# Kernel optimization log

Hardware: AMD Instinct MI355X
Metric: run time of the kernel (lower is better)

## Reference

```python
import jax, jax.numpy as jnp
import numpy as np
from jax import lax

BN_EPS = 1e-5

def _conv1d_same(x, w):
    # x: [N, 1, C], w: [1, 1, k] with k odd -> SAME padding along channel axis
    k = w.shape[-1]
    return lax.conv_general_dilated(x, w, window_strides=(1,),
                                    padding=[(k // 2, k // 2)],
                                    dimension_numbers=('NCH', 'OIH', 'NCH'))

def setup_inputs() -> dict:
    key = jax.random.key(0)
    ks = jax.random.split(key, 6)
    B, C, H, W = 4, 64, 64, 64
    kk = 3  # kernel size from in_dim=64: t=int(abs(log2(64)+1)/2)=3 (odd)
    x = jax.random.normal(ks[0], (B, C, H, W), dtype=jnp.float32)
    q_w = jax.random.normal(ks[1], (1, 1, kk), dtype=jnp.float32) * 0.5
    k_w = jax.random.normal(ks[2], (1, 1, kk), dtype=jnp.float32) * 0.5
    v_w = jax.random.normal(ks[3], (C, C), dtype=jnp.float32) * (1.0 / np.sqrt(C))
    v_b = jnp.zeros((C,), dtype=jnp.float32)
    gamma = jax.random.uniform(ks[4], (1,), dtype=jnp.float32, minval=0.5, maxval=1.5)
    bn_w = jnp.ones((C,), dtype=jnp.float32)
    bn_b = jnp.zeros((C,), dtype=jnp.float32)
    return {"x": x, "q_w": q_w, "k_w": k_w, "v_w": v_w, "v_b": v_b,
            "gamma": gamma, "bn_w": bn_w, "bn_b": bn_b}

def reference(x, q_w, k_w, v_w, v_b, gamma, bn_w, bn_b):
    B, C, H, W = x.shape
    N = H * W
    # conv1d Q/K projections over the channel axis, per spatial position
    xp = x.reshape(B, C, N).transpose(0, 2, 1).reshape(B * N, 1, C)
    q = _conv1d_same(xp, q_w).reshape(B, N, C)   # proj_query: [B, HW, C]
    k = _conv1d_same(xp, k_w).reshape(B, N, C)   # proj_key (pre-permute)
    energy = jnp.einsum('bnc,bmc->bnm', q, k)    # [B, HW, HW]
    attn = jax.nn.softmax(energy, axis=-1)
    # 1x1 value conv
    v = jnp.einsum('oc,bchw->bohw', v_w, x) + v_b[None, :, None, None]
    vv = v.reshape(B, C, N)
    # bmm(value, attention^T)
    out = jnp.einsum('bcm,bnm->bcn', vv, attn).reshape(B, C, H, W)
    y = gamma[0] * out
    # BatchNorm2d, training mode (batch statistics, biased variance)
    mean = jnp.mean(y, axis=(0, 2, 3), keepdims=True)
    var = jnp.var(y, axis=(0, 2, 3), keepdims=True)
    y = (y - mean) * lax.rsqrt(var + BN_EPS)
    y = y * bn_w[None, :, None, None] + bn_b[None, :, None, None]
    return y + x
```

## Files before the change

kernel.cpp:

```cpp
#include <hip/hip_runtime.h>
#include <stdint.h>

using f16 = _Float16;

typedef _Float16 f16x8 __attribute__((ext_vector_type(8)));
typedef _Float16 f16x4 __attribute__((ext_vector_type(4)));
typedef float f32x4 __attribute__((ext_vector_type(4)));

#define LOG2E 1.44269504088896340736f

__device__ __forceinline__ f16 f2h(float f) { return (f16)f; }

#if __has_builtin(__builtin_amdgcn_exp2f)
__device__ __forceinline__ float fexp2(float x) { return __builtin_amdgcn_exp2f(x); }
#else
__device__ __forceinline__ float fexp2(float x) { return exp2f(x); }
#endif

typedef __attribute__((address_space(1))) const uint32_t gu32;
typedef __attribute__((address_space(3))) uint32_t lu32;

__device__ __forceinline__ void dma16(const void* g, void* l) {
  __builtin_amdgcn_global_load_lds((gu32*)g, (lu32*)l, 16, 0, 0);
}

__device__ __forceinline__ f16x8 cvt8(const float* p) {
  const float4 a = *(const float4*)p;
  const float4 b = *(const float4*)(p + 4);
  f16x8 r;
  r[0] = (f16)a.x; r[1] = (f16)a.y; r[2] = (f16)a.z; r[3] = (f16)a.w;
  r[4] = (f16)b.x; r[5] = (f16)b.y; r[6] = (f16)b.z; r[7] = (f16)b.w;
  return r;
}


__global__ __launch_bounds__(256, 2) void pam_pre(
    const float* __restrict__ x, const float* __restrict__ qw,
    const float* __restrict__ kw, const float* __restrict__ vw,
    const float* __restrict__ vb,
    f16* __restrict__ qa, f16* __restrict__ ka2, f16* __restrict__ va3,
    float* __restrict__ gz)
{
  __shared__ alignas(16) f16 xt[16 * 72];
  const int tid = threadIdx.x;
  const int b = blockIdx.x >> 8;
  const int n0 = (blockIdx.x & 255) << 4;
  const int lane = tid & 63;
  const int wv = tid >> 6;
  const int quad = lane >> 4, l15 = lane & 15;

  if (blockIdx.x == 0 && tid < 128) gz[tid] = 0.f;

  {
    const int c = tid >> 2;
    const int j0 = (tid & 3) << 2;
    const float4 v0 = *(const float4*)(x + ((size_t)(b * 64 + c) << 12) + n0 + j0);
    xt[(j0 + 0) * 72 + c] = f2h(v0.x);
    xt[(j0 + 1) * 72 + c] = f2h(v0.y);
    xt[(j0 + 2) * 72 + c] = f2h(v0.z);
    xt[(j0 + 3) * 72 + c] = f2h(v0.w);
  }
  __syncthreads();

  const float qw0 = qw[0], qw1 = qw[1], qw2 = qw[2];
  const float kw0 = kw[0], kw1 = kw[1], kw2 = kw[2];
  for (int p = 0; p < 4; ++p) {
    const int c = lane;
    const int jr = (p << 2) + wv;
    const int n = n0 + jr;
    const float xm = (c > 0) ? (float)xt[jr * 72 + c - 1] : 0.f;
    const float x0 = (float)xt[jr * 72 + c];
    const float xp = (c < 63) ? (float)xt[jr * 72 + c + 1] : 0.f;
    const float qv = (qw0 * xm + qw1 * x0 + qw2 * xp) * LOG2E;
    const float kv = kw0 * xm + kw1 * x0 + kw2 * xp;
    qa[((size_t)((b << 12) + n) << 6) + c] = f2h(qv);
    ka2[((size_t)(b * 8 + (c >> 3)) << 15) + (n << 3) + (c & 7)] = f2h(kv);
  }

  {
    const f16x8 a0 = cvt8(vw + (wv * 16 + l15) * 64 + quad * 8);
    const f16x8 a1 = cvt8(vw + (wv * 16 + l15) * 64 + quad * 8 + 32);
    const f16x8 b0 = *(const f16x8*)&xt[l15 * 72 + quad * 8];
    const f16x8 b1 = *(const f16x8*)&xt[l15 * 72 + quad * 8 + 32];
    f32x4 z = {0.f, 0.f, 0.f, 0.f};
    z = __builtin_amdgcn_mfma_f32_16x16x32_f16(a0, b0, z, 0, 0, 0);
    z = __builtin_amdgcn_mfma_f32_16x16x32_f16(a1, b1, z, 0, 0, 0);
    const int cobase = wv * 16 + quad * 4;
    for (int r = 0; r < 4; ++r) {
      const int co = cobase + r;
      const int n = n0 + l15;
      const float val = z[r] + vb[co];
      va3[(((size_t)(b * 1024 + (n >> 2))) << 8) + (co << 2) + (n & 3)] = f2h(val);
    }
  }
}

__global__ __launch_bounds__(512, 2) void pam_attn(
    const f16* __restrict__ qa, const f16* __restrict__ ka2,
    const f16* __restrict__ va3, const float* __restrict__ gam,
    float* __restrict__ y0, float* __restrict__ gs1, float* __restrict__ gs2)
{
  __shared__ alignas(16) f16 kbuf[2][8192];
  __shared__ alignas(16) f16 vbuf[2][8192];
  __shared__ float ldsO[32 * 65];
  __shared__ float ldsM[4][32], ldsL[4][32], ldsMg[32], ldsInv[32];

  const int tid = threadIdx.x;
  const int wv = tid >> 6, lane = tid & 63;
  const int quad = lane >> 4, l15 = lane & 15;
  const int ks = wv & 3, qh = wv >> 2;
  const int b = blockIdx.x & 3;
  const int qb = blockIdx.x >> 2;
  const int qb0 = qb << 5;
  const int phase = qb & 31;

  for (int i = tid; i < 32 * 65; i += 512) ldsO[i] = 0.f;

  const int bn = b << 12;
  f16x8 bq0, bq1;
  {
    const int q = qb0 + qh * 16 + l15;
    const f16* qp = qa + ((size_t)(bn + q) << 6) + quad * 8;
    bq0 = *(const f16x8*)qp;
    bq1 = *(const f16x8*)(qp + 32);
  }

  const f16* kg0 = ka2 + (((size_t)(b * 8 + wv)) << 15) + (lane << 3);
  const f16* vg0 = va3 + ((size_t)b << 18) + (wv << 10) + (lane << 3);

  f32x4 o[4] = {};
  float m = -1e30f, lp = 0.f;

  dma16(kg0 + ((size_t)phase << 10),       kbuf[0] + (wv << 10));
  dma16(kg0 + ((size_t)phase << 10) + 512, kbuf[0] + (wv << 10) + 512);
  dma16(vg0 + ((size_t)phase << 13),       vbuf[0] + (wv << 10));
  dma16(vg0 + ((size_t)phase << 13) + 512, vbuf[0] + (wv << 10) + 512);
  __syncthreads();

#pragma unroll 1
  for (int kt = 0; kt < 32; ++kt) {
    const int cur = kt & 1;
    {
      const int tn = (kt + 1 + phase) & 31;
      f16* kd = kbuf[cur ^ 1] + (wv << 10);
      f16* vd = vbuf[cur ^ 1] + (wv << 10);
      dma16(kg0 + ((size_t)tn << 10),       kd);
      dma16(kg0 + ((size_t)tn << 10) + 512, kd + 512);
      dma16(vg0 + ((size_t)tn << 13),       vd);
      dma16(vg0 + ((size_t)tn << 13) + 512, vd + 512);
    }

    const f16* kc = kbuf[cur];
    const f16* vc = vbuf[cur];
    const int keyL0 = (ks * 32 + l15) << 3;
    const int keyL1 = (ks * 32 + 16 + l15) << 3;
    const f16x8 ak00 = *(const f16x8*)(kc + quad * 1024 + keyL0);
    const f16x8 ak01 = *(const f16x8*)(kc + (4 + quad) * 1024 + keyL0);
    const f16x8 ak10 = *(const f16x8*)(kc + quad * 1024 + keyL1);
    const f16x8 ak11 = *(const f16x8*)(kc + (4 + quad) * 1024 + keyL1);

    f32x4 s0, s1;
    {
      f32x4 z = {0.f, 0.f, 0.f, 0.f};
      z = __builtin_amdgcn_mfma_f32_16x16x32_f16(ak00, bq0, z, 0, 0, 0);
      s0 = __builtin_amdgcn_mfma_f32_16x16x32_f16(ak01, bq1, z, 0, 0, 0);
    }
    {
      f32x4 z = {0.f, 0.f, 0.f, 0.f};
      z = __builtin_amdgcn_mfma_f32_16x16x32_f16(ak10, bq0, z, 0, 0, 0);
      s1 = __builtin_amdgcn_mfma_f32_16x16x32_f16(ak11, bq1, z, 0, 0, 0);
    }

    float tmax = fmaxf(fmaxf(fmaxf(s0[0], s0[1]), fmaxf(s0[2], s0[3])),
                       fmaxf(fmaxf(s1[0], s1[1]), fmaxf(s1[2], s1[3])));
    tmax = fmaxf(tmax, __shfl_xor(tmax, 16, 64));
    tmax = fmaxf(tmax, __shfl_xor(tmax, 32, 64));
    const bool upd = tmax > m;
    const float mnew = upd ? tmax : m;

    f16x4 a0, a1;
    float tsum = 0.f;
    {
      const float p0 = fexp2(s0[0] - mnew);
      const float p1 = fexp2(s0[1] - mnew);
      const float p2 = fexp2(s0[2] - mnew);
      const float p3 = fexp2(s0[3] - mnew);
      tsum += (p0 + p1) + (p2 + p3);
      a0[0] = f2h(p0); a0[1] = f2h(p1); a0[2] = f2h(p2); a0[3] = f2h(p3);
    }
    {
      const float p0 = fexp2(s1[0] - mnew);
      const float p1 = fexp2(s1[1] - mnew);
      const float p2 = fexp2(s1[2] - mnew);
      const float p3 = fexp2(s1[3] - mnew);
      tsum += (p0 + p1) + (p2 + p3);
      a1[0] = f2h(p0); a1[1] = f2h(p1); a1[2] = f2h(p2); a1[3] = f2h(p3);
    }

    if (__any(upd)) {
      const float alpha = fexp2(m - mnew);
      lp = lp * alpha + tsum;
      const int srcbase = (lane & 48) + ((lane >> 4) << 2);
      for (int r = 0; r < 4; ++r) {
        const float ar = __shfl(alpha, srcbase + r, 64);
        for (int ct = 0; ct < 4; ++ct) o[ct][r] *= ar;
      }
    } else {
      lp += tsum;
    }
    m = mnew;

    for (int ct = 0; ct < 4; ++ct) {
      const int cb = (ct * 16 + l15) << 2;
      const f16x4 bv0 = *(const f16x4*)(vc + ((ks * 8 + quad) << 8) + cb);
      const f16x4 bv1 = *(const f16x4*)(vc + ((ks * 8 + 4 + quad) << 8) + cb);
      o[ct] = __builtin_amdgcn_mfma_f32_16x16x16f16(a0, bv0, o[ct], 0, 0, 0);
      o[ct] = __builtin_amdgcn_mfma_f32_16x16x16f16(a1, bv1, o[ct], 0, 0, 0);
    }
    __syncthreads();
  }

  {
    float v = lp;
    v += __shfl_xor(v, 16, 64);
    v += __shfl_xor(v, 32, 64);
    if (quad == 0) {
      ldsM[ks][qh * 16 + l15] = m;
      ldsL[ks][qh * 16 + l15] = v;
    }
  }
  __syncthreads();

  if (tid < 32) {
    const float M = fmaxf(fmaxf(ldsM[0][tid], ldsM[1][tid]),
                          fmaxf(ldsM[2][tid], ldsM[3][tid]));
    const float lt = ldsL[0][tid] * fexp2(ldsM[0][tid] - M) +
                     ldsL[1][tid] * fexp2(ldsM[1][tid] - M) +
                     ldsL[2][tid] * fexp2(ldsM[2][tid] - M) +
                     ldsL[3][tid] * fexp2(ldsM[3][tid] - M);
    ldsMg[tid] = M;
    ldsInv[tid] = 1.f / lt;
  }
  __syncthreads();

  for (int r = 0; r < 4; ++r) {
    const int q = qh * 16 + quad * 4 + r;
    const float sc = fexp2(ldsM[ks][q] - ldsMg[q]);
    for (int ct = 0; ct < 4; ++ct)
      atomicAdd(&ldsO[q * 65 + ct * 16 + l15], o[ct][r] * sc);
  }
  __syncthreads();

  const float g = gam[0];
  {
    const int c = tid >> 3;
    const int q0 = (tid & 7) << 2;
    float4 v4;
    float* vp = &v4.x;
    float s1 = 0.f, s2 = 0.f;
    for (int r = 0; r < 4; ++r) {
      const float val = g * ldsO[(q0 + r) * 65 + c] * ldsInv[q0 + r];
      vp[r] = val; s1 += val; s2 += val * val;
    }
    *(float4*)(y0 + ((size_t)(b * 64 + c) << 12) + qb0 + q0) = v4;
    s1 += __shfl_xor(s1, 1, 64);
    s2 += __shfl_xor(s2, 1, 64);
    s1 += __shfl_xor(s1, 2, 64);
    s2 += __shfl_xor(s2, 2, 64);
    s1 += __shfl_xor(s1, 4, 64);
    s2 += __shfl_xor(s2, 4, 64);
    if ((tid & 7) == 0) {
      atomicAdd(&gs1[c], s1);
      atomicAdd(&gs2[c], s2);
    }
  }
}

__global__ __launch_bounds__(256, 2) void pam_apply(
    const float* __restrict__ y0, const float* __restrict__ x,
    const float* __restrict__ gs1, const float* __restrict__ gs2,
    const float* __restrict__ bnw, const float* __restrict__ bnb,
    float* __restrict__ out)
{
  const int i = (blockIdx.x * 256 + threadIdx.x) << 2;
  const int c = (i >> 12) & 63;
  const float inv_n = 1.f / 16384.f;
  const float mean = gs1[c] * inv_n;
  const float var = fmaxf(gs2[c] * inv_n - mean * mean, 0.f);
  const float sc = bnw[c] * rsqrtf(var + 1e-5f);
  const float sh = bnb[c] - mean * sc;
  const float4 y = *(const float4*)(y0 + i);
  const float4 xv = *(const float4*)(x + i);
  float4 r;
  r.x = y.x * sc + sh + xv.x;
  r.y = y.y * sc + sh + xv.y;
  r.z = y.z * sc + sh + xv.z;
  r.w = y.w * sc + sh + xv.w;
  *(float4*)(out + i) = r;
}

extern "C" void kernel_launch(void* const* d_in, const int* in_sizes, int n_in,
                              void* d_out, int out_size, void* d_ws, size_t ws_size,
                              hipStream_t stream)
{
  (void)in_sizes; (void)n_in; (void)out_size; (void)ws_size;
  const float* x   = (const float*)d_in[0];
  const float* qw  = (const float*)d_in[1];
  const float* kw  = (const float*)d_in[2];
  const float* vw  = (const float*)d_in[3];
  const float* vb  = (const float*)d_in[4];
  const float* gam = (const float*)d_in[5];
  const float* bnw = (const float*)d_in[6];
  const float* bnb = (const float*)d_in[7];

  char* ws = (char*)d_ws;
  f16*   qa  = (f16*)(ws);
  f16*   ka2 = (f16*)(ws + (2u << 20));
  f16*   va3 = (f16*)(ws + (4u << 20));
  float* y0  = (float*)(ws + (6u << 20));
  float* gs1 = (float*)(ws + (10u << 20));
  float* gs2 = (float*)(ws + (10u << 20) + 256);

  pam_pre  <<<1024, 256, 0, stream>>>(x, qw, kw, vw, vb, qa, ka2, va3, gs1);
  pam_attn <<<512, 512, 0, stream>>>(qa, ka2, va3, gam, y0, gs1, gs2);
  pam_apply<<<1024, 256, 0, stream>>>(y0, x, gs1, gs2, bnw, bnb, (float*)d_out);
}
```

Before: 153.6 us.

## Restructure attention to 32x32 MFMA with direct register loads and lazy rescale

Rewrites the attention kernel so each 1024-thread block handles 64 queries across 8 key-split waves, using 32x32x16 MFMA tiles. K and V are loaded straight from global memory into registers (K prefetched one tile ahead) instead of being staged through double-buffered LDS with per-iteration barriers. The value layout in the pre kernel changes to match. The online-softmax max update is now skipped unless the tile max exceeds the running max by more than 8, and MFMA issue priority is raised. The changes aim to remove LDS round-trips and syncs and to raise MFMA efficiency, at the cost of more register pressure, more global traffic per wave, and half as many blocks.

```diff
diff --git a/kernel.cpp b/kernel.cpp
--- a/kernel.cpp
+++ b/kernel.cpp
@@ -4,8 +4,8 @@
 using f16 = _Float16;
 
 typedef _Float16 f16x8 __attribute__((ext_vector_type(8)));
-typedef _Float16 f16x4 __attribute__((ext_vector_type(4)));
 typedef float f32x4 __attribute__((ext_vector_type(4)));
+typedef float f32x16 __attribute__((ext_vector_type(16)));
 
 #define LOG2E 1.44269504088896340736f
 
@@ -16,13 +16,6 @@
 #else
 __device__ __forceinline__ float fexp2(float x) { return exp2f(x); }
 #endif
-
-typedef __attribute__((address_space(1))) const uint32_t gu32;
-typedef __attribute__((address_space(3))) uint32_t lu32;
-
-__device__ __forceinline__ void dma16(const void* g, void* l) {
-  __builtin_amdgcn_global_load_lds((gu32*)g, (lu32*)l, 16, 0, 0);
-}
 
 __device__ __forceinline__ f16x8 cvt8(const float* p) {
   const float4 a = *(const float4*)p;
@@ -90,188 +83,161 @@
       const int co = cobase + r;
       const int n = n0 + l15;
       const float val = z[r] + vb[co];
-      va3[(((size_t)(b * 1024 + (n >> 2))) << 8) + (co << 2) + (n & 3)] = f2h(val);
-    }
-  }
-}
-
-__global__ __launch_bounds__(512, 2) void pam_attn(
+      va3[(((size_t)(b * 512 + (n >> 3))) << 9) + (co << 3) + (n & 7)] = f2h(val);
+    }
+  }
+}
+
+__global__ __launch_bounds__(1024, 4) void pam_attn(
     const f16* __restrict__ qa, const f16* __restrict__ ka2,
     const f16* __restrict__ va3, const float* __restrict__ gam,
     float* __restrict__ y0, float* __restrict__ gs1, float* __restrict__ gs2)
 {
-  __shared__ alignas(16) f16 kbuf[2][8192];
-  __shared__ alignas(16) f16 vbuf[2][8192];
-  __shared__ float ldsO[32 * 65];
-  __shared__ float ldsM[4][32], ldsL[4][32], ldsMg[32], ldsInv[32];
+  __shared__ alignas(16) float ldsO[2][64][32];
+  __shared__ float ldsM[2][8][32], ldsL[2][8][32];
+  __shared__ float ldsInv[2][32];
 
   const int tid = threadIdx.x;
-  const int wv = tid >> 6, lane = tid & 63;
-  const int quad = lane >> 4, l15 = lane & 15;
-  const int ks = wv & 3, qh = wv >> 2;
-  const int b = blockIdx.x & 3;
-  const int qb = blockIdx.x >> 2;
-  const int qb0 = qb << 5;
-  const int phase = qb & 31;
-
-  for (int i = tid; i < 32 * 65; i += 512) ldsO[i] = 0.f;
-
-  const int bn = b << 12;
-  f16x8 bq0, bq1;
-  {
-    const int q = qb0 + qh * 16 + l15;
-    const f16* qp = qa + ((size_t)(bn + q) << 6) + quad * 8;
-    bq0 = *(const f16x8*)qp;
-    bq1 = *(const f16x8*)(qp + 32);
-  }
-
-  const f16* kg0 = ka2 + (((size_t)(b * 8 + wv)) << 15) + (lane << 3);
-  const f16* vg0 = va3 + ((size_t)b << 18) + (wv << 10) + (lane << 3);
-
-  f32x4 o[4] = {};
+  const int lane = tid & 63, wv = tid >> 6;
+  const int qg = wv >> 3, ks = wv & 7;
+  const int q = lane & 31, hi = lane >> 5;
+  const int slot = (int)blockIdx.x & 7, tt = (int)blockIdx.x >> 3;
+  const int b = slot >> 1;
+  const int qb0 = ((tt << 1) | (slot & 1)) << 6;
+  const int qbase = qb0 + (qg << 5);
+
+  {
+    float* z0 = (float*)ldsO;
+    for (int i = tid; i < 2 * 64 * 32; i += 1024) z0[i] = 0.f;
+  }
+
+  f16x8 bq0, bq1, bq2, bq3;
+  {
+    const f16* qp = qa + (((size_t)((b << 12) + qbase + q)) << 6) + (hi << 3);
+    bq0 = *(const f16x8*)(qp);
+    bq1 = *(const f16x8*)(qp + 16);
+    bq2 = *(const f16x8*)(qp + 32);
+    bq3 = *(const f16x8*)(qp + 48);
+  }
+
+  const int gq = (q & 0x13) | ((q & 4) << 1) | ((q & 8) >> 1);
+  const f16* kp0 = ka2 + (((size_t)(b * 8 + hi)) << 15) + (ks << 12) + (gq << 3);
+  const f16* vp0 = va3 + (((size_t)(b * 512 + ks * 64 + hi)) << 9) + (q << 3);
+
+  f32x16 oc0 = {}, oc1 = {};
   float m = -1e30f, lp = 0.f;
 
-  dma16(kg0 + ((size_t)phase << 10),       kbuf[0] + (wv << 10));
-  dma16(kg0 + ((size_t)phase << 10) + 512, kbuf[0] + (wv << 10) + 512);
-  dma16(vg0 + ((size_t)phase << 13),       vbuf[0] + (wv << 10));
-  dma16(vg0 + ((size_t)phase << 13) + 512, vbuf[0] + (wv << 10) + 512);
+  f16x8 k0 = *(const f16x8*)(kp0);
+  f16x8 k1 = *(const f16x8*)(kp0 + 65536);
+  f16x8 k2 = *(const f16x8*)(kp0 + 131072);
+  f16x8 k3 = *(const f16x8*)(kp0 + 196608);
+
+#pragma unroll 2
+  for (int kt = 0; kt < 16; ++kt) {
+    const f16* vp = vp0 + (kt << 11);
+    const f16x8 v00 = *(const f16x8*)(vp);
+    const f16x8 v01 = *(const f16x8*)(vp + 256);
+    const f16x8 v10 = *(const f16x8*)(vp + 1024);
+    const f16x8 v11 = *(const f16x8*)(vp + 1280);
+
+    f32x16 z = {};
+    __builtin_amdgcn_s_setprio(1);
+    z = __builtin_amdgcn_mfma_f32_32x32x16_f16(k0, bq0, z, 0, 0, 0);
+    z = __builtin_amdgcn_mfma_f32_32x32x16_f16(k1, bq1, z, 0, 0, 0);
+    z = __builtin_amdgcn_mfma_f32_32x32x16_f16(k2, bq2, z, 0, 0, 0);
+    z = __builtin_amdgcn_mfma_f32_32x32x16_f16(k3, bq3, z, 0, 0, 0);
+    __builtin_amdgcn_s_setprio(0);
+
+    if (kt < 15) {
+      const f16* kp = kp0 + ((kt + 1) << 8);
+      k0 = *(const f16x8*)(kp);
+      k1 = *(const f16x8*)(kp + 65536);
+      k2 = *(const f16x8*)(kp + 131072);
+      k3 = *(const f16x8*)(kp + 196608);
+    }
+
+    float t0 = fmaxf(fmaxf(z[0], z[1]), fmaxf(z[2], z[3]));
+    float t1 = fmaxf(fmaxf(z[4], z[5]), fmaxf(z[6], z[7]));
+    float t2 = fmaxf(fmaxf(z[8], z[9]), fmaxf(z[10], z[11]));
+    float t3 = fmaxf(fmaxf(z[12], z[13]), fmaxf(z[14], z[15]));
+    float tmax = fmaxf(fmaxf(t0, t1), fmaxf(t2, t3));
+    tmax = fmaxf(tmax, __shfl_xor(tmax, 32, 64));
+    const bool need = !__all(tmax <= m + 8.f);
+    const float mn = need ? fmaxf(m, tmax) : m;
+
+    float p[16];
+#pragma unroll
+    for (int j = 0; j < 16; ++j) p[j] = fexp2(z[j] - mn);
+    float s0 = (p[0] + p[1]) + (p[2] + p[3]);
+    float s1 = (p[4] + p[5]) + (p[6] + p[7]);
+    float s2 = (p[8] + p[9]) + (p[10] + p[11]);
+    float s3 = (p[12] + p[13]) + (p[14] + p[15]);
+    const float ts = (s0 + s1) + (s2 + s3);
+
+    f16x8 pa0, pa1;
+#pragma unroll
+    for (int j = 0; j < 8; ++j) { pa0[j] = f2h(p[j]); pa1[j] = f2h(p[j + 8]); }
+
+    if (need) {
+      const float al = fexp2(m - mn);
+      lp = lp * al + ts;
+      m = mn;
+#pragma unroll
+      for (int j = 0; j < 16; ++j) { oc0[j] *= al; oc1[j] *= al; }
+    } else {
+      lp += ts;
+    }
+
+    __builtin_amdgcn_s_setprio(1);
+    oc0 = __builtin_amdgcn_mfma_f32_32x32x16_f16(v00, pa0, oc0, 0, 0, 0);
+    oc0 = __builtin_amdgcn_mfma_f32_32x32x16_f16(v10, pa1, oc0, 0, 0, 0);
+    oc1 = __builtin_amdgcn_mfma_f32_32x32x16_f16(v01, pa0, oc1, 0, 0, 0);
+    oc1 = __builtin_amdgcn_mfma_f32_32x32x16_f16(v11, pa1, oc1, 0, 0, 0);
+    __builtin_amdgcn_s_setprio(0);
+  }
+
+  lp += __shfl_xor(lp, 32, 64);
+  if (hi == 0) { ldsM[qg][ks][q] = m; ldsL[qg][ks][q] = lp; }
   __syncthreads();
 
-#pragma unroll 1
-  for (int kt = 0; kt < 32; ++kt) {
-    const int cur = kt & 1;
-    {
-      const int tn = (kt + 1 + phase) & 31;
-      f16* kd = kbuf[cur ^ 1] + (wv << 10);
-      f16* vd = vbuf[cur ^ 1] + (wv << 10);
-      dma16(kg0 + ((size_t)tn << 10),       kd);
-      dma16(kg0 + ((size_t)tn << 10) + 512, kd + 512);
-      dma16(vg0 + ((size_t)tn << 13),       vd);
-      dma16(vg0 + ((size_t)tn << 13) + 512, vd + 512);
-    }
-
-    const f16* kc = kbuf[cur];
-    const f16* vc = vbuf[cur];
-    const int keyL0 = (ks * 32 + l15) << 3;
-    const int keyL1 = (ks * 32 + 16 + l15) << 3;
-    const f16x8 ak00 = *(const f16x8*)(kc + quad * 1024 + keyL0);
-    const f16x8 ak01 = *(const f16x8*)(kc + (4 + quad) * 1024 + keyL0);
-    const f16x8 ak10 = *(const f16x8*)(kc + quad * 1024 + keyL1);
-    const f16x8 ak11 = *(const f16x8*)(kc + (4 + quad) * 1024 + keyL1);
-
-    f32x4 s0, s1;
-    {
-      f32x4 z = {0.f, 0.f, 0.f, 0.f};
-      z = __builtin_amdgcn_mfma_f32_16x16x32_f16(ak00, bq0, z, 0, 0, 0);
-      s0 = __builtin_amdgcn_mfma_f32_16x16x32_f16(ak01, bq1, z, 0, 0, 0);
-    }
-    {
-      f32x4 z = {0.f, 0.f, 0.f, 0.f};
-      z = __builtin_amdgcn_mfma_f32_16x16x32_f16(ak10, bq0, z, 0, 0, 0);
-      s1 = __builtin_amdgcn_mfma_f32_16x16x32_f16(ak11, bq1, z, 0, 0, 0);
-    }
-
-    float tmax = fmaxf(fmaxf(fmaxf(s0[0], s0[1]), fmaxf(s0[2], s0[3])),
-                       fmaxf(fmaxf(s1[0], s1[1]), fmaxf(s1[2], s1[3])));
-    tmax = fmaxf(tmax, __shfl_xor(tmax, 16, 64));
-    tmax = fmaxf(tmax, __shfl_xor(tmax, 32, 64));
-    const bool upd = tmax > m;
-    const float mnew = upd ? tmax : m;
-
-    f16x4 a0, a1;
-    float tsum = 0.f;
-    {
-      const float p0 = fexp2(s0[0] - mnew);
-      const float p1 = fexp2(s0[1] - mnew);
-      const float p2 = fexp2(s0[2] - mnew);
-      const float p3 = fexp2(s0[3] - mnew);
-      tsum += (p0 + p1) + (p2 + p3);
-      a0[0] = f2h(p0); a0[1] = f2h(p1); a0[2] = f2h(p2); a0[3] = f2h(p3);
-    }
-    {
-      const float p0 = fexp2(s1[0] - mnew);
-      const float p1 = fexp2(s1[1] - mnew);
-      const float p2 = fexp2(s1[2] - mnew);
-      const float p3 = fexp2(s1[3] - mnew);
-      tsum += (p0 + p1) + (p2 + p3);
-      a1[0] = f2h(p0); a1[1] = f2h(p1); a1[2] = f2h(p2); a1[3] = f2h(p3);
-    }
-
-    if (__any(upd)) {
-      const float alpha = fexp2(m - mnew);
-      lp = lp * alpha + tsum;
-      const int srcbase = (lane & 48) + ((lane >> 4) << 2);
-      for (int r = 0; r < 4; ++r) {
-        const float ar = __shfl(alpha, srcbase + r, 64);
-        for (int ct = 0; ct < 4; ++ct) o[ct][r] *= ar;
-      }
-    } else {
-      lp += tsum;
-    }
-    m = mnew;
-
-    for (int ct = 0; ct < 4; ++ct) {
-      const int cb = (ct * 16 + l15) << 2;
-      const f16x4 bv0 = *(const f16x4*)(vc + ((ks * 8 + quad) << 8) + cb);
-      const f16x4 bv1 = *(const f16x4*)(vc + ((ks * 8 + 4 + quad) << 8) + cb);
-      o[ct] = __builtin_amdgcn_mfma_f32_16x16x16f16(a0, bv0, o[ct], 0, 0, 0);
-      o[ct] = __builtin_amdgcn_mfma_f32_16x16x16f16(a1, bv1, o[ct], 0, 0, 0);
-    }
-    __syncthreads();
-  }
-
-  {
-    float v = lp;
-    v += __shfl_xor(v, 16, 64);
-    v += __shfl_xor(v, 32, 64);
-    if (quad == 0) {
-      ldsM[ks][qh * 16 + l15] = m;
-      ldsL[ks][qh * 16 + l15] = v;
-    }
+  float M = ldsM[qg][0][q];
+#pragma unroll
+  for (int k = 1; k < 8; ++k) M = fmaxf(M, ldsM[qg][k][q]);
+  float lt = 0.f;
+#pragma unroll
+  for (int k = 0; k < 8; ++k) lt += ldsL[qg][k][q] * fexp2(ldsM[qg][k][q] - M);
+  if (ks == 0 && hi == 0) ldsInv[qg][q] = 1.f / lt;
+  const float sc = fexp2(m - M);
+
+#pragma unroll
+  for (int t = 0; t < 16; ++t) {
+    const int c0 = (t & 3) + ((t >> 2) << 3) + (hi << 2);
+    atomicAdd(&ldsO[qg][c0][q], oc0[t] * sc);
+    atomicAdd(&ldsO[qg][c0 + 32][q], oc1[t] * sc);
   }
   __syncthreads();
 
-  if (tid < 32) {
-    const float M = fmaxf(fmaxf(ldsM[0][tid], ldsM[1][tid]),
-                          fmaxf(ldsM[2][tid], ldsM[3][tid]));
-    const float lt = ldsL[0][tid] * fexp2(ldsM[0][tid] - M) +
-                     ldsL[1][tid] * fexp2(ldsM[1][tid] - M) +
-                     ldsL[2][tid] * fexp2(ldsM[2][tid] - M) +
-                     ldsL[3][tid] * fexp2(ldsM[3][tid] - M);
-    ldsMg[tid] = M;
-    ldsInv[tid] = 1.f / lt;
-  }
-  __syncthreads();
-
-  for (int r = 0; r < 4; ++r) {
-    const int q = qh * 16 + quad * 4 + r;
-    const float sc = fexp2(ldsM[ks][q] - ldsMg[q]);
-    for (int ct = 0; ct < 4; ++ct)
-      atomicAdd(&ldsO[q * 65 + ct * 16 + l15], o[ct][r] * sc);
-  }
-  __syncthreads();
-
   const float g = gam[0];
   {
-    const int c = tid >> 3;
+    const int qg2 = tid >> 9;
+    const int c = (tid >> 3) & 63;
     const int q0 = (tid & 7) << 2;
+    const int nn = qb0 + (qg2 << 5) + q0;
     float4 v4;
-    float* vp = &v4.x;
-    float s1 = 0.f, s2 = 0.f;
+    float* vp4 = &v4.x;
+    float b1 = 0.f, b2 = 0.f;
+#pragma unroll
     for (int r = 0; r < 4; ++r) {
-      const float val = g * ldsO[(q0 + r) * 65 + c] * ldsInv[q0 + r];
-      vp[r] = val; s1 += val; s2 += val * val;
-    }
-    *(float4*)(y0 + ((size_t)(b * 64 + c) << 12) + qb0 + q0) = v4;
-    s1 += __shfl_xor(s1, 1, 64);
-    s2 += __shfl_xor(s2, 1, 64);
-    s1 += __shfl_xor(s1, 2, 64);
-    s2 += __shfl_xor(s2, 2, 64);
-    s1 += __shfl_xor(s1, 4, 64);
-    s2 += __shfl_xor(s2, 4, 64);
+      const float val = g * ldsO[qg2][c][q0 + r] * ldsInv[qg2][q0 + r];
+      vp4[r] = val; b1 += val; b2 += val * val;
+    }
+    *(float4*)(y0 + (((size_t)(b * 64 + c)) << 12) + nn) = v4;
+    b1 += __shfl_xor(b1, 1, 64); b2 += __shfl_xor(b2, 1, 64);
+    b1 += __shfl_xor(b1, 2, 64); b2 += __shfl_xor(b2, 2, 64);
+    b1 += __shfl_xor(b1, 4, 64); b2 += __shfl_xor(b2, 4, 64);
     if ((tid & 7) == 0) {
-      atomicAdd(&gs1[c], s1);
-      atomicAdd(&gs2[c], s2);
+      atomicAdd(&gs1[c], b1);
+      atomicAdd(&gs2[c], b2);
     }
   }
 }
@@ -322,6 +288,6 @@
   float* gs2 = (float*)(ws + (10u << 20) + 256);
 
   pam_pre  <<<1024, 256, 0, stream>>>(x, qw, kw, vw, vb, qa, ka2, va3, gs1);
-  pam_attn <<<512, 512, 0, stream>>>(qa, ka2, va3, gam, y0, gs1, gs2);
+  pam_attn <<<256, 1024, 0, stream>>>(qa, ka2, va3, gam, y0, gs1, gs2);
   pam_apply<<<1024, 256, 0, stream>>>(y0, x, gs1, gs2, bnw, bnb, (float*)d_out);
 }
```

Result: slower. 169.3 us (+10.3%).

## Transpose PV MFMA to use 16x16x32 with per-lane rescale and lazy max

Applied to the files above, without the earlier changes.

Changes the V layout to 8-key groups and permutes the key ordering so the probability tile can feed the PV product directly as the B operand of a 16x16x32 MFMA, halving the PV MFMA count per tile. The output accumulator is now transposed (query per lane column), so the rescale no longer needs cross-lane shuffles of alpha. It also adds a lazy max update with a threshold of 8, so rescaling is skipped unless the running max grows substantially, at the cost of larger exponent ranges in fp16 probabilities. The final LDS merge is adjusted to the new accumulator orientation.

```diff
diff --git a/kernel.cpp b/kernel.cpp
--- a/kernel.cpp
+++ b/kernel.cpp
@@ -90,7 +90,7 @@
       const int co = cobase + r;
       const int n = n0 + l15;
       const float val = z[r] + vb[co];
-      va3[(((size_t)(b * 1024 + (n >> 2))) << 8) + (co << 2) + (n & 3)] = f2h(val);
+      va3[(((size_t)(b * 512 + (n >> 3))) << 9) + (co << 3) + (n & 7)] = f2h(val);
     }
   }
 }
@@ -136,6 +136,11 @@
   dma16(vg0 + ((size_t)phase << 13),       vbuf[0] + (wv << 10));
   dma16(vg0 + ((size_t)phase << 13) + 512, vbuf[0] + (wv << 10) + 512);
   __syncthreads();
+
+  const int kperm = (ks << 5) + (((l15 >> 2) << 3) | (l15 & 3));
+  const int koff0 = kperm << 3;
+  const int koff1 = (kperm + 4) << 3;
+  const int vbase = ((ks * 4 + quad) << 9) + (l15 << 3);
 
 #pragma unroll 1
   for (int kt = 0; kt < 32; ++kt) {
@@ -152,70 +157,60 @@
 
     const f16* kc = kbuf[cur];
     const f16* vc = vbuf[cur];
-    const int keyL0 = (ks * 32 + l15) << 3;
-    const int keyL1 = (ks * 32 + 16 + l15) << 3;
-    const f16x8 ak00 = *(const f16x8*)(kc + quad * 1024 + keyL0);
-    const f16x8 ak01 = *(const f16x8*)(kc + (4 + quad) * 1024 + keyL0);
-    const f16x8 ak10 = *(const f16x8*)(kc + quad * 1024 + keyL1);
-    const f16x8 ak11 = *(const f16x8*)(kc + (4 + quad) * 1024 + keyL1);
-
-    f32x4 s0, s1;
+    const f16x8 ak00 = *(const f16x8*)(kc + (quad << 10) + koff0);
+    const f16x8 ak01 = *(const f16x8*)(kc + ((4 + quad) << 10) + koff0);
+    const f16x8 ak10 = *(const f16x8*)(kc + (quad << 10) + koff1);
+    const f16x8 ak11 = *(const f16x8*)(kc + ((4 + quad) << 10) + koff1);
+
+    f32x4 z0, z1;
     {
       f32x4 z = {0.f, 0.f, 0.f, 0.f};
       z = __builtin_amdgcn_mfma_f32_16x16x32_f16(ak00, bq0, z, 0, 0, 0);
-      s0 = __builtin_amdgcn_mfma_f32_16x16x32_f16(ak01, bq1, z, 0, 0, 0);
+      z0 = __builtin_amdgcn_mfma_f32_16x16x32_f16(ak01, bq1, z, 0, 0, 0);
     }
     {
       f32x4 z = {0.f, 0.f, 0.f, 0.f};
       z = __builtin_amdgcn_mfma_f32_16x16x32_f16(ak10, bq0, z, 0, 0, 0);
-      s1 = __builtin_amdgcn_mfma_f32_16x16x32_f16(ak11, bq1, z, 0, 0, 0);
-    }
-
-    float tmax = fmaxf(fmaxf(fmaxf(s0[0], s0[1]), fmaxf(s0[2], s0[3])),
-                       fmaxf(fmaxf(s1[0], s1[1]), fmaxf(s1[2], s1[3])));
+      s1_label:
+      z1 = __builtin_amdgcn_mfma_f32_16x16x32_f16(ak11, bq1, z, 0, 0, 0);
+    }
+
+    float tmax = fmaxf(fmaxf(fmaxf(z0[0], z0[1]), fmaxf(z0[2], z0[3])),
+                       fmaxf(fmaxf(z1[0], z1[1]), fmaxf(z1[2], z1[3])));
     tmax = fmaxf(tmax, __shfl_xor(tmax, 16, 64));
     tmax = fmaxf(tmax, __shfl_xor(tmax, 32, 64));
-    const bool upd = tmax > m;
-    const float mnew = upd ? tmax : m;
-
-    f16x4 a0, a1;
-    float tsum = 0.f;
-    {
-      const float p0 = fexp2(s0[0] - mnew);
-      const float p1 = fexp2(s0[1] - mnew);
-      const float p2 = fexp2(s0[2] - mnew);
-      const float p3 = fexp2(s0[3] - mnew);
-      tsum += (p0 + p1) + (p2 + p3);
-      a0[0] = f2h(p0); a0[1] = f2h(p1); a0[2] = f2h(p2); a0[3] = f2h(p3);
-    }
-    {
-      const float p0 = fexp2(s1[0] - mnew);
-      const float p1 = fexp2(s1[1] - mnew);
-      const float p2 = fexp2(s1[2] - mnew);
-      const float p3 = fexp2(s1[3] - mnew);
-      tsum += (p0 + p1) + (p2 + p3);
-      a1[0] = f2h(p0); a1[1] = f2h(p1); a1[2] = f2h(p2); a1[3] = f2h(p3);
-    }
-
-    if (__any(upd)) {
-      const float alpha = fexp2(m - mnew);
-      lp = lp * alpha + tsum;
-      const int srcbase = (lane & 48) + ((lane >> 4) << 2);
-      for (int r = 0; r < 4; ++r) {
-        const float ar = __shfl(alpha, srcbase + r, 64);
-        for (int ct = 0; ct < 4; ++ct) o[ct][r] *= ar;
-      }
+    const bool need = !__all(tmax <= m + 8.f);
+    const float mn = need ? fmaxf(m, tmax) : m;
+
+    const float p0 = fexp2(z0[0] - mn);
+    const float p1 = fexp2(z0[1] - mn);
+    const float p2 = fexp2(z0[2] - mn);
+    const float p3 = fexp2(z0[3] - mn);
+    const float p4 = fexp2(z1[0] - mn);
+    const float p5 = fexp2(z1[1] - mn);
+    const float p6 = fexp2(z1[2] - mn);
+    const float p7 = fexp2(z1[3] - mn);
+    const float ts = ((p0 + p1) + (p2 + p3)) + ((p4 + p5) + (p6 + p7));
+
+    f16x8 pa;
+    pa[0] = f2h(p0); pa[1] = f2h(p1); pa[2] = f2h(p2); pa[3] = f2h(p3);
+    pa[4] = f2h(p4); pa[5] = f2h(p5); pa[6] = f2h(p6); pa[7] = f2h(p7);
+
+    if (need) {
+      const float al = fexp2(m - mn);
+      lp = lp * al + ts;
+      m = mn;
+#pragma unroll
+      for (int ct = 0; ct < 4; ++ct)
+        for (int r = 0; r < 4; ++r) o[ct][r] *= al;
     } else {
-      lp += tsum;
-    }
-    m = mnew;
-
+      lp += ts;
+    }
+
+#pragma unroll
     for (int ct = 0; ct < 4; ++ct) {
-      const int cb = (ct * 16 + l15) << 2;
-      const f16x4 bv0 = *(const f16x4*)(vc + ((ks * 8 + quad) << 8) + cb);
-      const f16x4 bv1 = *(const f16x4*)(vc + ((ks * 8 + 4 + quad) << 8) + cb);
-      o[ct] = __builtin_amdgcn_mfma_f32_16x16x16f16(a0, bv0, o[ct], 0, 0, 0);
-      o[ct] = __builtin_amdgcn_mfma_f32_16x16x16f16(a1, bv1, o[ct], 0, 0, 0);
+      const f16x8 av = *(const f16x8*)(vc + vbase + ct * 128);
+      o[ct] = __builtin_amdgcn_mfma_f32_16x16x32_f16(av, pa, o[ct], 0, 0, 0);
     }
     __syncthreads();
   }
@@ -243,11 +238,13 @@
   }
   __syncthreads();
 
-  for (int r = 0; r < 4; ++r) {
-    const int q = qh * 16 + quad * 4 + r;
-    const float sc = fexp2(ldsM[ks][q] - ldsMg[q]);
+  {
+    const int q = qh * 16 + l15;
+    const float sc = fexp2(m - ldsMg[q]);
+#pragma unroll
     for (int ct = 0; ct < 4; ++ct)
-      atomicAdd(&ldsO[q * 65 + ct * 16 + l15], o[ct][r] * sc);
+      for (int r = 0; r < 4; ++r)
+        atomicAdd(&ldsO[q * 65 + ct * 16 + quad * 4 + r], o[ct][r] * sc);
   }
   __syncthreads();
 
```

Measured after the change: 149.7 us. 2.5% less time.
